# Kernel tuning notes

Hardware: AMD Instinct MI355X
Metric: run time of the kernel (lower is better)

Reference implementation:

```python
import jax, jax.numpy as jnp
import numpy as np

HS = 512; L = 4; T = 128; M = 2048; FF = 2048; NH = 4; DH = HS // NH
STDV = 1.0 / float(np.sqrt(HS))


def setup_inputs() -> dict:
    key = jax.random.key(0)
    ks = iter(jax.random.split(key, 32))

    def u(shape):
        return jax.random.uniform(next(ks), shape, jnp.float32, -STDV, STDV)

    return {
        "x": jax.random.normal(next(ks), (1, T, HS), jnp.float32),
        "historical_states": jax.random.normal(next(ks), (M, L, HS), jnp.float32),
        "Wx": u((L, 3, HS, HS)), "bx": u((L, 3, HS)),
        "Wh": u((L, 3, HS, HS)), "bh": u((L, 3, HS)),
        "sa_Win": u((L, 3 * HS, HS)), "sa_bin": u((L, 3 * HS)),
        "sa_Wo": u((L, HS, HS)), "sa_bo": u((L, HS)),
        "ca_Win": u((L, 3 * HS, HS)), "ca_bin": u((L, 3 * HS)),
        "ca_Wo": u((L, HS, HS)), "ca_bo": u((L, HS)),
        "ff_W1": u((L, FF, HS)), "ff_b1": u((L, FF)),
        "ff_W2": u((L, HS, FF)), "ff_b2": u((L, HS)),
        "ln_g": u((L, 3, HS)), "ln_b": u((L, 3, HS)),
    }


def _layer_norm(v, g, b):
    m = v.mean(-1, keepdims=True)
    var = ((v - m) ** 2).mean(-1, keepdims=True)
    return (v - m) / jnp.sqrt(var + 1e-5) * g + b


def _forward(x, historical_states, Wx, bx, Wh, bh, sa_Win, sa_bin, sa_Wo, sa_bo,
             ca_Win, ca_bin, ca_Wo, ca_bo, ff_W1, ff_b1, ff_W2, ff_b2, ln_g, ln_b):
    n_layers, _, hs, _ = Wx.shape
    # Cross-attn K/V over the static historical memory are time-invariant: precompute once.
    Wk = ca_Win[:, hs:2 * hs, :]; bk = ca_bin[:, hs:2 * hs]
    Wv = ca_Win[:, 2 * hs:, :]; bv = ca_bin[:, 2 * hs:]
    K = (jnp.einsum('mle,lfe->lmf', historical_states, Wk) + bk[:, None, :]).reshape(n_layers, -1, NH, DH)
    V = (jnp.einsum('mle,lfe->lmf', historical_states, Wv) + bv[:, None, :]).reshape(n_layers, -1, NH, DH)
    scale = 1.0 / jnp.sqrt(jnp.asarray(DH, x.dtype))

    def decoder(i, f):
        # post-norm TransformerDecoderLayer, tgt length 1, eval mode (no dropout).
        # Self-attn over a single position: softmax of one logit == 1 -> out = Wo @ (Wv_self f + bv_self) + bo.
        v_sa = sa_Win[i, 2 * hs:] @ f + sa_bin[i, 2 * hs:]
        sa = sa_Wo[i] @ v_sa + sa_bo[i]
        x1 = _layer_norm(f + sa, ln_g[i, 0], ln_b[i, 0])
        q = (ca_Win[i, :hs] @ x1 + ca_bin[i, :hs]).reshape(NH, DH)
        att = jax.nn.softmax(jnp.einsum('hd,mhd->hm', q, K[i]) * scale, axis=-1)
        ctx = jnp.einsum('hm,mhd->hd', att, V[i]).reshape(hs)
        x2 = _layer_norm(x1 + ca_Wo[i] @ ctx + ca_bo[i], ln_g[i, 1], ln_b[i, 1])
        ff = ff_W2[i] @ jax.nn.relu(ff_W1[i] @ x2 + ff_b1[i]) + ff_b2[i]
        return _layer_norm(x2 + ff, ln_g[i, 2], ln_b[i, 2])

    def step(carry, x_t):
        h_prev, c_prev = carry  # (L, HS) each; batch is structurally 1
        xin = x_t
        h_new = []; c_new = []
        for i in range(n_layers):
            z = (jnp.einsum('gij,j->gi', Wx[i], xin) + bx[i]
                 + jnp.einsum('gij,j->gi', Wh[i], h_prev[i]) + bh[i])  # (3, HS)
            i_t = jax.nn.sigmoid(z[0]); f0 = jax.nn.sigmoid(z[1]); g_t = jnp.tanh(z[2])
            f_t = jax.nn.sigmoid(c_prev[i] - decoder(i, f0))
            c_i = f_t * c_prev[i] + i_t * g_t
            xin = jnp.tanh(c_i)
            h_new.append(xin); c_new.append(c_i)
        h = jnp.stack(h_new); c = jnp.stack(c_new)
        return (h, c), h[-1]

    h0 = jnp.zeros((n_layers, hs), x.dtype)
    c0 = jnp.zeros((n_layers, hs), x.dtype)
    (h_T, c_T), hidden = jax.lax.scan(step, (h0, c0), x[0])  # hidden: (T, HS)
    return hidden[None], h_T[:, None, :], c_T[:, None, :]


def reference(x, historical_states, Wx, bx, Wh, bh, sa_Win, sa_bin, sa_Wo, sa_bo,
              ca_Win, ca_bin, ca_Wo, ca_bo, ff_W1, ff_b1, ff_W2, ff_b2, ln_g, ln_b):
    return _forward(x, historical_states, Wx, bx, Wh, bh, sa_Win, sa_bin, sa_Wo, sa_bo,
                    ca_Win, ca_bin, ca_Wo, ca_bo, ff_W1, ff_b1, ff_W2, ff_b2, ln_g, ln_b)
```

## Files before the change

### kernel.cpp

```cpp
#include <hip/hip_runtime.h>

#define HS   512
#define LNUM 4
#define TT   128
#define MMEM 2048
#define FFD  2048
#define NB   256
#define NT   512
#define INV512 (1.0f/512.0f)
#define QSCALE 0.08838834764831845f

constexpr size_t KHALF = (size_t)LNUM*MMEM*HS/2;
constexpr size_t HHALF = (size_t)LNUM*HS*HS/2;
constexpr size_t FHALF = (size_t)LNUM*FFD*HS/2;
constexpr size_t OFF_KBF    = 0;
constexpr size_t OFF_VBF    = OFF_KBF    + KHALF;
constexpr size_t OFF_WCOMBBF= OFF_VBF    + KHALF;
constexpr size_t OFF_WQTBF  = OFF_WCOMBBF+ HHALF;
constexpr size_t OFF_W2TBF  = OFF_WQTBF  + HHALF;
constexpr size_t OFF_FFW1BF = OFF_W2TBF  + FHALF;
constexpr size_t OFF_CAWOBF = OFF_FFW1BF + FHALF;
constexpr size_t OFF_CSA    = OFF_CAWOBF + HHALF;
constexpr size_t OFF_SQ     = OFF_CSA    + (size_t)LNUM*HS;
constexpr size_t OFF_CBQ    = OFF_SQ     + (size_t)LNUM*HS;
constexpr size_t OFF_STATE = OFF_CBQ   + (size_t)LNUM*HS;
constexpr size_t OFF_H     = OFF_STATE;
constexpr size_t OFF_C     = OFF_H     + 2*LNUM*HS;
constexpr size_t OFF_XING  = OFF_C     + 2*LNUM*HS;
constexpr size_t OFF_Z1    = OFF_XING  + HS;
constexpr size_t OFF_Z02   = OFF_Z1    + HS;
constexpr size_t OFF_T2G   = OFF_Z02   + 2*HS;
constexpr size_t OFF_YP    = OFF_T2G   + HS;
constexpr size_t OFF_Y2P   = OFF_YP    + 4*HS;
constexpr size_t OFF_CTXP  = OFF_Y2P   + 8*HS;
constexpr size_t OFF_DENS  = OFF_CTXP  + 8*HS;
constexpr size_t OFF_S1S   = OFF_DENS  + 128;
constexpr size_t OFF_S2S   = OFF_S1S   + 64;
constexpr size_t OFF_J1    = OFF_S2S   + 64;
constexpr size_t OFF_J2    = OFF_J1    + 65*32;
constexpr size_t OFF_FLAGS = OFF_J2    + 128*32;
constexpr size_t WS_TOTAL  = OFF_FLAGS + (size_t)NB*32;

__device__ __forceinline__ float wred(float v) {
#pragma unroll
  for (int m = 32; m; m >>= 1) v += __shfl_xor(v, m);
  return v;
}
__device__ __forceinline__ float sigm(float x) { return 1.0f/(1.0f+__expf(-x)); }

__device__ __forceinline__ unsigned short f2bf(float f) {
  unsigned u = __float_as_uint(f);
  unsigned r = (u + 0x7fffu + ((u >> 16) & 1u)) >> 16;
  return (unsigned short)r;
}
__device__ __forceinline__ float bf2f(unsigned short h) {
  return __uint_as_float(((unsigned)h) << 16);
}

__device__ __forceinline__ float ald(const float* p) {
  return __hip_atomic_load(p, __ATOMIC_RELAXED, __HIP_MEMORY_SCOPE_AGENT);
}
__device__ __forceinline__ void ast(float* p, float v) {
  __hip_atomic_store(p, v, __ATOMIC_RELAXED, __HIP_MEMORY_SCOPE_AGENT);
}
__device__ __forceinline__ unsigned aldu(const unsigned* p) {
  return __hip_atomic_load(p, __ATOMIC_RELAXED, __HIP_MEMORY_SCOPE_AGENT);
}
__device__ __forceinline__ void astu(unsigned* p, unsigned v) {
  __hip_atomic_store(p, v, __ATOMIC_RELAXED, __HIP_MEMORY_SCOPE_AGENT);
}

template <class F>
__device__ __forceinline__ void barrier_pf(unsigned* flags, unsigned g, F&& pf) {
  asm volatile("s_waitcnt vmcnt(0)" ::: "memory");
  __syncthreads();
  if (threadIdx.x == 0) astu(flags + (size_t)blockIdx.x*32, g);
  pf();
  if (threadIdx.x < NB) {
    const unsigned* f = flags + (size_t)threadIdx.x*32;
    while ((int)(aldu(f) - g) < 0) __builtin_amdgcn_s_sleep(2);
  }
  __syncthreads();
}

__device__ __forceinline__ void jflag(unsigned* J, int id, unsigned val) {
  asm volatile("s_waitcnt vmcnt(0)" ::: "memory");
  __syncthreads();
  if (threadIdx.x == 0) astu(J + (size_t)id*32, val);
}
template <class F>
__device__ __forceinline__ void jwait_pf(unsigned* J, int n, unsigned val, F&& pf) {
  pf();
  if (threadIdx.x < n) {
    const unsigned* f = J + (size_t)threadIdx.x*32;
    while ((int)(aldu(f) - val) < 0) __builtin_amdgcn_s_sleep(1);
  }
  __syncthreads();
}

__device__ __forceinline__ void slotred32(const float* slots, float* sh, int o,
                                          int w, int lane) {
  if (w == 0) {
    float a = (lane < 32) ? ald(slots + lane*2) : ald(slots + (lane-32)*2 + 1);
#pragma unroll
    for (int m = 16; m; m >>= 1) a += __shfl_xor(a, m);
    if (lane == 0)  sh[o]   = a;
    if (lane == 32) sh[o+1] = a;
  }
}


__global__ __launch_bounds__(256) void kv_gemm(
    const float* __restrict__ hist, const float* __restrict__ caWin,
    const float* __restrict__ caBin, unsigned short* __restrict__ out, int koff) {
  __shared__ float As[16][64];
  __shared__ float Bs[16][64];
  const int l = blockIdx.z, m0 = blockIdx.x*64, f0 = blockIdx.y*64;
  const int tid = threadIdx.x, tm = tid >> 4, tf = tid & 15;
  float acc[4][4] = {};
  for (int e0 = 0; e0 < HS; e0 += 16) {
#pragma unroll
    for (int it = 0; it < 4; ++it) {
      int idx = tid + it*256, k = idx & 15, mm = idx >> 4;
      As[k][mm] = hist[((size_t)(m0+mm)*LNUM + l)*HS + e0 + k];
      Bs[k][mm] = caWin[((size_t)l*(3*HS) + koff + f0 + mm)*HS + e0 + k];
    }
    __syncthreads();
#pragma unroll
    for (int k = 0; k < 16; ++k) {
      float a[4], b[4];
#pragma unroll
      for (int x = 0; x < 4; ++x) { a[x] = As[k][tm*4+x]; b[x] = Bs[k][tf*4+x]; }
#pragma unroll
      for (int x = 0; x < 4; ++x)
#pragma unroll
        for (int y = 0; y < 4; ++y) acc[x][y] += a[x]*b[y];
    }
    __syncthreads();
  }
#pragma unroll
  for (int x = 0; x < 4; ++x)
#pragma unroll
    for (int y = 0; y < 4; ++y) {
      int m = m0 + tm*4 + x, f = f0 + tf*4 + y;
      out[((size_t)l*MMEM + m)*HS + f] = f2bf(acc[x][y] + caBin[l*(3*HS) + koff + f]);
    }
}

__global__ __launch_bounds__(256) void wcomb_gemm(
    const float* __restrict__ saWo, const float* __restrict__ saWin,
    unsigned short* __restrict__ wcomb) {
  __shared__ float As[16][64];
  __shared__ float Bs[16][64];
  const int l = blockIdx.z, f0 = blockIdx.x*64, j0 = blockIdx.y*64;
  const int tid = threadIdx.x, tm = tid >> 4, tf = tid & 15;
  float acc[4][4] = {};
  for (int e0 = 0; e0 < HS; e0 += 16) {
#pragma unroll
    for (int it = 0; it < 4; ++it) {
      int idx = tid + it*256;
      { int k = idx & 15, ff = idx >> 4;
        As[k][ff] = saWo[((size_t)l*HS + f0+ff)*HS + e0 + k]; }
      { int jj = idx & 63, k = idx >> 6;
        Bs[k][jj] = saWin[((size_t)l*(3*HS) + 2*HS + e0 + k)*HS + j0 + jj]; }
    }
    __syncthreads();
#pragma unroll
    for (int k = 0; k < 16; ++k) {
      float a[4], b[4];
#pragma unroll
      for (int x = 0; x < 4; ++x) { a[x] = As[k][tm*4+x]; b[x] = Bs[k][tf*4+x]; }
#pragma unroll
      for (int x = 0; x < 4; ++x)
#pragma unroll
        for (int y = 0; y < 4; ++y) acc[x][y] += a[x]*b[y];
    }
    __syncthreads();
  }
#pragma unroll
  for (int x = 0; x < 4; ++x)
#pragma unroll
    for (int y = 0; y < 4; ++y)
      wcomb[(size_t)l*HS*HS + (size_t)(f0+tm*4+x)*HS + (j0+tf*4+y)] = f2bf(acc[x][y]);
}

__global__ __launch_bounds__(256) void transpose_scale_bf(
    const float* __restrict__ in, size_t inLS, int R, int C,
    const float* __restrict__ g, size_t gLS,
    unsigned short* __restrict__ out, size_t outLS) {
  __shared__ float tile[32][33];
  const int l = blockIdx.z, e0 = blockIdx.x*32, f0 = blockIdx.y*32;
  const int tx = threadIdx.x & 31, ty = threadIdx.x >> 5;
#pragma unroll
  for (int r = 0; r < 32; r += 8)
    tile[ty+r][tx] = in[(size_t)l*inLS + (size_t)(f0+ty+r)*C + e0 + tx];
  __syncthreads();
#pragma unroll
  for (int r = 0; r < 32; r += 8) {
    int e = e0 + ty + r, f = f0 + tx;
    float s = g ? g[(size_t)l*gLS + e] : 1.0f;
    out[(size_t)l*outLS + (size_t)e*R + f] = f2bf(tile[tx][ty+r] * s);
  }
}

__global__ __launch_bounds__(256) void bf16_copy(
    const float* __restrict__ in, unsigned short* __restrict__ out, size_t n) {
  for (size_t i = (size_t)blockIdx.x*256 + threadIdx.x; i < n; i += (size_t)gridDim.x*256)
    out[i] = f2bf(in[i]);
}

__global__ __launch_bounds__(256) void csa_kernel(
    const float* __restrict__ saWo, const float* __restrict__ sabin,
    const float* __restrict__ sabo, float* __restrict__ csa) {
  const int w = threadIdx.x >> 6, lane = threadIdx.x & 63;
  const int row = blockIdx.x*4 + w;
  const int l = row >> 9, f = row & 511;
  float acc = 0;
#pragma unroll
  for (int k = 0; k < 8; ++k) {
    int e = lane + 64*k;
    acc += saWo[((size_t)l*HS + f)*HS + e] * sabin[l*(3*HS) + 2*HS + e];
  }
  acc = wred(acc);
  if (lane == 0) csa[row] = acc + sabo[l*HS + f];
}

__global__ __launch_bounds__(256) void sqcbq_kernel(
    const float* __restrict__ caWin, const float* __restrict__ caBin,
    const float* __restrict__ lnG, const float* __restrict__ lnB,
    float* __restrict__ sq, float* __restrict__ cbq) {
  const int w = threadIdx.x >> 6, lane = threadIdx.x & 63;
  const int row = blockIdx.x*4 + w;
  const int l = row >> 9, f = row & 511;
  float a1 = 0, a2 = 0;
#pragma unroll
  for (int k = 0; k < 8; ++k) {
    int e = lane + 64*k;
    float wv = caWin[((size_t)l*(3*HS) + f)*HS + e];
    a1 += wv * lnG[l*(3*HS) + e];
    a2 += wv * lnB[l*(3*HS) + e];
  }
  a1 = wred(a1); a2 = wred(a2);
  if (lane == 0) { sq[row] = a1; cbq[row] = a2 + caBin[l*(3*HS) + f]; }
}


__global__ __launch_bounds__(NT, 2) void seq_kernel(
    const float* __restrict__ x,
    const float* __restrict__ Wx,  const float* __restrict__ bx,
    const float* __restrict__ Wh,  const float* __restrict__ bh,
    const float* __restrict__ caBo,
    const float* __restrict__ ffB1,
    const float* __restrict__ ffB2,
    const float* __restrict__ lnG,  const float* __restrict__ lnB,
    float* __restrict__ ws, float* __restrict__ out) {
  const unsigned short* Kb    = (const unsigned short*)(ws + OFF_KBF);
  const unsigned short* Vb    = (const unsigned short*)(ws + OFF_VBF);
  const unsigned short* Wcomb = (const unsigned short*)(ws + OFF_WCOMBBF);
  const unsigned short* WqT   = (const unsigned short*)(ws + OFF_WQTBF);
  const unsigned short* W2T   = (const unsigned short*)(ws + OFF_W2TBF);
  const unsigned short* F1b   = (const unsigned short*)(ws + OFF_FFW1BF);
  const unsigned short* CaWob = (const unsigned short*)(ws + OFF_CAWOBF);
  const float* csag  = ws + OFF_CSA;
  const float* sqg   = ws + OFF_SQ;
  const float* cbqg  = ws + OFF_CBQ;
  float* hG    = ws + OFF_H;
  float* cG    = ws + OFF_C;
  float* xing  = ws + OFF_XING;
  float* z1g   = ws + OFF_Z1;
  float* z02g  = ws + OFF_Z02;
  float* t2g   = ws + OFF_T2G;
  float* Yp    = ws + OFF_YP;
  float* Y2p   = ws + OFF_Y2P;
  float* ctxP  = ws + OFF_CTXP;
  float* denS  = ws + OFF_DENS;
  float* s1s   = ws + OFF_S1S;
  float* s2s   = ws + OFF_S2S;
  unsigned* J1     = (unsigned*)(ws + OFF_J1);
  unsigned* J2     = (unsigned*)(ws + OFF_J2);
  unsigned* bflags = (unsigned*)(ws + OFF_FLAGS);

  __shared__ float sh_xin[HS], sh_h[HS], sh_vec[HS], sh_aux[HS];
  __shared__ float sh_q[128], sh_p[64], sh_t1[16];
  __shared__ float sh_red[24], sh_den[4];

  const int bid = blockIdx.x, tid = threadIdx.x;
  const int w = tid >> 6, lane = tid & 63;
  unsigned gen = 1;

  float pZx[8], pZh[8];
  float pZx2[8], pZh2[8];
  unsigned short pWc[2][8], pWq[16];
  unsigned short pK[8][2], pV[16];
  unsigned short pCa[2][8];
  unsigned short pF1[8], pW2[8];

  auto pfH1 = [&](int l) {
    if (bid < 64) {
      const float* wxr = Wx + (((size_t)l*3 + 1)*HS + bid*8 + w)*HS;
      const float* whr = Wh + (((size_t)l*3 + 1)*HS + bid*8 + w)*HS;
#pragma unroll
      for (int k = 0; k < 8; ++k) { pZx[k] = wxr[lane+64*k]; pZh[k] = whr[lane+64*k]; }
    }
  };
  auto pfH2 = [&](int l) {
    if (bid < 32) {
#pragma unroll
      for (int rr = 0; rr < 2; ++rr) {
        const unsigned short* wr = Wcomb + ((size_t)l*HS + bid*16 + w*2 + rr)*HS;
#pragma unroll
        for (int k = 0; k < 8; ++k) pWc[rr][k] = wr[lane+64*k];
      }
#pragma unroll
      for (int r = 0; r < 16; ++r)
        pWq[r] = WqT[((size_t)l*HS + bid*16 + r)*HS + tid];
    }
  };
  auto pfH3 = [&](int l) {
    if (bid >= 32 && bid < 160) {
      const int b2 = bid - 32, h = b2 >> 5, mseg = b2 & 31;
#pragma unroll
      for (int rr = 0; rr < 8; ++rr) {
        const unsigned short* kr = Kb + ((size_t)l*MMEM + mseg*64 + w*8 + rr)*HS + h*128;
        pK[rr][0] = kr[lane]; pK[rr][1] = kr[lane+64];
      }
#pragma unroll
      for (int ml = 0; ml < 16; ++ml)
        pV[ml] = Vb[((size_t)l*MMEM + mseg*64 + (tid>>7)*16 + ml)*HS + h*128 + (tid & 127)];
    }
  };
  auto pfZ = [&](int l) {
    if (bid < 32 || bid >= 160) {
      const int zb = (bid < 32) ? bid : bid - 128;
      const int rowid = zb*8 + w;
      const int g = (rowid < 512) ? 0 : 2;
      const int f = rowid & 511;
      const float* wxr = Wx + (((size_t)l*3 + g)*HS + f)*HS;
      const float* whr = Wh + (((size_t)l*3 + g)*HS + f)*HS;
#pragma unroll
      for (int k = 0; k < 8; ++k) { pZx2[k] = wxr[lane+64*k]; pZh2[k] = whr[lane+64*k]; }
    }
  };
  auto pfH4 = [&](int l) {
    if (bid < 32) {
#pragma unroll
      for (int rr = 0; rr < 2; ++rr) {
        const unsigned short* wr = CaWob + ((size_t)l*HS + bid*16 + w*2 + rr)*HS;
#pragma unroll
        for (int k = 0; k < 8; ++k) pCa[rr][k] = wr[lane+64*k];
      }
    }
  };
  auto pfH5 = [&](int l) {
    const unsigned short* wr = F1b + ((size_t)l*FFD + bid*8 + w)*HS;
#pragma unroll
    for (int k = 0; k < 8; ++k) pF1[k] = wr[lane+64*k];
#pragma unroll
    for (int r = 0; r < 8; ++r)
      pW2[r] = W2T[((size_t)l*FFD + bid*8 + r)*HS + tid];
  };

  auto do_update = [&](int ip, int parp, float& xn, float& cn) {
    const int j = tid;
    float t2v = ald(t2g + j);
    float z0  = ald(z02g + j);
    float z2  = ald(z02g + HS + j);
    float y2 = 0;
#pragma unroll
    for (int p = 0; p < 8; ++p) y2 += ald(Y2p + (size_t)p*HS + j);
    slotred32(s2s, sh_red, 16, w, lane);
    __syncthreads();
    float m2 = sh_red[16]*INV512;
    float r2 = rsqrtf(sh_red[17]*INV512 - m2*m2 + 1e-5f);
    float x2 = (t2v-m2)*r2*lnG[(ip*3+1)*HS+j] + lnB[(ip*3+1)*HS+j];
    float t3 = x2 + y2 + ffB2[ip*HS + j];
    float s_ = t3, q_ = t3*t3;
#pragma unroll
    for (int m = 32; m; m >>= 1) { s_ += __shfl_xor(s_, m); q_ += __shfl_xor(q_, m); }
    if (lane == 0) { sh_red[w] = s_; sh_red[8+w] = q_; }
    __syncthreads();
    if (tid == 0) {
      float a = 0, b = 0;
#pragma unroll
      for (int k = 0; k < 8; ++k) { a += sh_red[k]; b += sh_red[8+k]; }
      sh_red[0] = a; sh_red[1] = b;
    }
    __syncthreads();
    float m3 = sh_red[0]*INV512;
    float r3 = rsqrtf(sh_red[1]*INV512 - m3*m3 + 1e-5f);
    float d  = (t3-m3)*r3*lnG[(ip*3+2)*HS+j] + lnB[(ip*3+2)*HS+j];
    float cp = ald(cG + (parp*LNUM + ip)*HS + j);
    float ft = sigm(cp - d);
    float it = sigm(z0);
    float gt = tanhf(z2);
    cn = ft*cp + it*gt;
    xn = tanhf(cn);
  };

  pfH1(0); pfH2(0); pfH3(0);

  for (int s = 0; s < TT*LNUM; ++s) {
    const int t = s >> 2, i = s & 3;
    const int par = t & 1;
    const unsigned jv = (unsigned)(s + 1);
    if (bid < 64) {
      float xn = 0.f, cn = 0.f;
      if (s > 0) {
        const int ip = (s-1) & 3, tp = (s-1) >> 2, parp = tp & 1;
        if (bid == 0 || i > 0) {
          do_update(ip, parp, xn, cn);
          if (bid == 0) {
            ast(hG + ((parp^1)*LNUM + ip)*HS + tid, xn);
            ast(cG + ((parp^1)*LNUM + ip)*HS + tid, cn);
            if (ip == 3) out[tp*HS + tid] = xn;
          }
        }
      }
      float xv = (i == 0) ? x[t*HS + tid] : xn;
      sh_xin[tid] = xv;
      sh_h[tid]   = ald(hG + (par*LNUM + i)*HS + tid);
      if (bid == 0) ast(xing + tid, xv);
      __syncthreads();
      const int f = bid*8 + w;
      float acc = 0;
#pragma unroll
      for (int k = 0; k < 8; ++k) {
        int e = lane + 64*k;
        acc += pZx[k]*sh_xin[e] + pZh[k]*sh_h[e];
      }
      acc = wred(acc);
      if (lane == 0) ast(z1g + f, acc + bx[(i*3+1)*HS + f] + bh[(i*3+1)*HS + f]);
      jflag(J1, bid, jv);
    } else if (bid == 64) {
#pragma unroll
      for (int p = 0; p < 4; ++p) ast(Yp + (size_t)p*HS + tid, 0.f);
      jflag(J1, 64, jv);
    } else if (bid == 65) {
#pragma unroll
      for (int p = 0; p < 8; ++p) ast(ctxP + (size_t)p*HS + tid, 0.f);
    } else if (bid == 66) {
      jwait_pf(J1, 65, jv, [&]{});
#pragma unroll
      for (int p = 0; p < 8; ++p) ast(Y2p + (size_t)p*HS + tid, 0.f);
    }
    if (bid < 32) {
      jwait_pf(J1, 65, jv, [&]{});
      sh_vec[tid] = sigm(ald(z1g + tid));
      __syncthreads();
#pragma unroll
      for (int rr = 0; rr < 2; ++rr) {
        const int r = w*2 + rr, j = bid*16 + r;
        float acc = 0;
#pragma unroll
        for (int k = 0; k < 8; ++k) acc += bf2f(pWc[rr][k])*sh_vec[lane + 64*k];
        acc = wred(acc);
        if (lane == 0) {
          float t1v = sh_vec[j] + acc + csag[i*HS + j];
          sh_t1[r]  = t1v;
          sh_aux[r] = t1v;
        }
      }
      __syncthreads();
      {
        float yl = 0;
#pragma unroll
        for (int r = 0; r < 16; ++r) yl += sh_aux[r] * bf2f(pWq[r]);
        atomicAdd(&Yp[(size_t)(bid & 3)*HS + tid], yl);
      }
      if (w == 0 && lane < 16) {
        float v = sh_aux[lane], s_ = v, q_ = v*v;
#pragma unroll
        for (int m = 8; m; m >>= 1) { s_ += __shfl_xor(s_, m); q_ += __shfl_xor(q_, m); }
        if (lane == 0) { ast(s1s + bid*2, s_); ast(s1s + bid*2 + 1, q_); }
      }
    }
    barrier_pf(bflags, gen, [&]{ pfZ(i); pfH4(i); pfH5(i); });
    if (bid >= 32 && bid < 160) {
      const int b2 = bid - 32, h = b2 >> 5, mseg = b2 & 31;
      slotred32(s1s, sh_red, 18, w, lane);
      __syncthreads();
      if (tid < 128) {
        float m1 = sh_red[18]*INV512;
        float r1 = rsqrtf(sh_red[19]*INV512 - m1*m1 + 1e-5f);
        int f = h*128 + tid;
        float Ysum = 0;
#pragma unroll
        for (int p = 0; p < 4; ++p) Ysum += ald(Yp + (size_t)p*HS + f);
        sh_q[tid] = r1*(Ysum - m1*sqg[i*HS + f]) + cbqg[i*HS + f];
      }
      __syncthreads();
#pragma unroll
      for (int rr = 0; rr < 8; ++rr) {
        float acc = sh_q[lane]*bf2f(pK[rr][0]) + sh_q[lane+64]*bf2f(pK[rr][1]);
        acc = wred(acc);
        if (lane == 0) sh_p[w*8 + rr] = __expf(acc * QSCALE);
      }
      __syncthreads();
      {
        const int d = tid & 127, mg = tid >> 7;
        float acc = 0;
#pragma unroll
        for (int ml = 0; ml < 16; ++ml) acc += sh_p[mg*16 + ml] * bf2f(pV[ml]);
        atomicAdd(&ctxP[(size_t)((b2 & 1)*4 + mg)*HS + h*128 + d], acc);
      }
      if (w == 0) {
        float v = wred(sh_p[lane]);
        if (lane == 0) ast(denS + h*32 + mseg, v);
      }
      jflag(J2, b2, jv);
    } else {
      const int zb = (bid < 32) ? bid : bid - 128;
      if (bid >= 160) {
        sh_xin[tid] = ald(xing + tid);
        sh_h[tid]   = ald(hG + (par*LNUM + i)*HS + tid);
      }
      __syncthreads();
      const int rowid = zb*8 + w;
      const int g = (rowid < 512) ? 0 : 2;
      const int f = rowid & 511;
      float acc = 0;
#pragma unroll
      for (int k = 0; k < 8; ++k) {
        int e = lane + 64*k;
        acc += pZx2[k]*sh_xin[e] + pZh2[k]*sh_h[e];
      }
      acc = wred(acc);
      if (lane == 0) ast(z02g + (g ? HS : 0) + f, acc + bx[(i*3+g)*HS + f] + bh[(i*3+g)*HS + f]);
      if (bid < 32) {
        jwait_pf(J2, 128, jv, [&]{});
        slotred32(s1s, sh_red, 18, w, lane);
        if (w >= 4) {
          float v = (lane < 32) ? ald(denS + (w-4)*32 + lane) : 0.f;
#pragma unroll
          for (int m = 16; m; m >>= 1) v += __shfl_xor(v, m);
          if (lane == 0) sh_den[w-4] = v;
        }
        __syncthreads();
        const float m1 = sh_red[18]*INV512;
        const float r1 = rsqrtf(sh_red[19]*INV512 - m1*m1 + 1e-5f);
        {
          float c = 0;
#pragma unroll
          for (int p = 0; p < 8; ++p) c += ald(ctxP + (size_t)p*HS + tid);
          sh_vec[tid] = c / sh_den[tid >> 7];
        }
        __syncthreads();
#pragma unroll
        for (int rr = 0; rr < 2; ++rr) {
          const int r = w*2 + rr, j = bid*16 + r;
          float a2 = 0;
#pragma unroll
          for (int k = 0; k < 8; ++k) a2 += bf2f(pCa[rr][k])*sh_vec[lane + 64*k];
          a2 = wred(a2);
          if (lane == 0) {
            float x1 = (sh_t1[r]-m1)*r1*lnG[(i*3)*HS + j] + lnB[(i*3)*HS + j];
            float t2v = x1 + a2 + caBo[i*HS + j];
            ast(t2g + j, t2v);
            sh_aux[r] = t2v;
          }
        }
        __syncthreads();
        if (w == 0 && lane < 16) {
          float v = sh_aux[lane], s_ = v, q_ = v*v;
#pragma unroll
          for (int m = 8; m; m >>= 1) { s_ += __shfl_xor(s_, m); q_ += __shfl_xor(q_, m); }
          if (lane == 0) { ast(s2s + bid*2, s_); ast(s2s + bid*2 + 1, q_); }
        }
      }
    }
    barrier_pf(bflags, gen+1, [&]{ const int nl = (s+1) & 3; pfH1(nl); pfH2(nl); pfH3(nl); });
    {
      slotred32(s2s, sh_red, 16, w, lane);
      __syncthreads();
      const float m2 = sh_red[16]*INV512;
      const float r2 = rsqrtf(sh_red[17]*INV512 - m2*m2 + 1e-5f);
      sh_vec[tid] = (ald(t2g + tid)-m2)*r2*lnG[(i*3+1)*HS + tid] + lnB[(i*3+1)*HS + tid];
      __syncthreads();
      const int kk = bid*8 + w;
      float acc = 0;
#pragma unroll
      for (int k = 0; k < 8; ++k) acc += bf2f(pF1[k])*sh_vec[lane + 64*k];
      acc = wred(acc);
      if (lane == 0) sh_aux[w] = fmaxf(acc + ffB1[i*FFD + kk], 0.f);
      __syncthreads();
      float yl = 0;
#pragma unroll
      for (int r = 0; r < 8; ++r) yl += sh_aux[r] * bf2f(pW2[r]);
      atomicAdd(&Y2p[(size_t)(bid & 7)*HS + tid], yl);
    }
    barrier_pf(bflags, gen+2, [&]{});
    gen += 3;
  }

  if (bid == 0) {
    float xn, cn;
    do_update(3, 1, xn, cn);
    out[127*HS + tid] = xn;
    out[TT*HS + 3*HS + tid] = xn;
    out[TT*HS + LNUM*HS + 3*HS + tid] = cn;
#pragma unroll
    for (int ii = 0; ii < 3; ++ii) {
      out[TT*HS + ii*HS + tid]            = ald(hG + (0*LNUM + ii)*HS + tid);
      out[TT*HS + LNUM*HS + ii*HS + tid]  = ald(cG + (0*LNUM + ii)*HS + tid);
    }
  }
}

extern "C" void kernel_launch(void* const* d_in, const int* in_sizes, int n_in,
                              void* d_out, int out_size, void* d_ws, size_t ws_size,
                              hipStream_t stream) {
  const float* x      = (const float*)d_in[0];
  const float* hist   = (const float*)d_in[1];
  const float* Wx     = (const float*)d_in[2];
  const float* bx     = (const float*)d_in[3];
  const float* Wh     = (const float*)d_in[4];
  const float* bh     = (const float*)d_in[5];
  const float* saWin  = (const float*)d_in[6];
  const float* saBin  = (const float*)d_in[7];
  const float* saWo   = (const float*)d_in[8];
  const float* saBo   = (const float*)d_in[9];
  const float* caWin  = (const float*)d_in[10];
  const float* caBin  = (const float*)d_in[11];
  const float* caWo   = (const float*)d_in[12];
  const float* caBo   = (const float*)d_in[13];
  const float* ffW1   = (const float*)d_in[14];
  const float* ffB1   = (const float*)d_in[15];
  const float* ffW2   = (const float*)d_in[16];
  const float* ffB2   = (const float*)d_in[17];
  const float* lnG    = (const float*)d_in[18];
  const float* lnB    = (const float*)d_in[19];
  float* ws  = (float*)d_ws;
  float* out = (float*)d_out;

  hipMemsetAsync((char*)d_ws + OFF_STATE*sizeof(float), 0,
                 (WS_TOTAL - OFF_STATE)*sizeof(float), stream);

  kv_gemm<<<dim3(MMEM/64, HS/64, LNUM), 256, 0, stream>>>(
      hist, caWin, caBin, (unsigned short*)(ws + OFF_KBF), HS);
  kv_gemm<<<dim3(MMEM/64, HS/64, LNUM), 256, 0, stream>>>(
      hist, caWin, caBin, (unsigned short*)(ws + OFF_VBF), 2*HS);
  wcomb_gemm<<<dim3(HS/64, HS/64, LNUM), 256, 0, stream>>>(
      saWo, saWin, (unsigned short*)(ws + OFF_WCOMBBF));
  csa_kernel<<<(LNUM*HS)/4, 256, 0, stream>>>(saWo, saBin, saBo, ws + OFF_CSA);
  transpose_scale_bf<<<dim3(HS/32, HS/32, LNUM), 256, 0, stream>>>(
      caWin, (size_t)(3*HS)*HS, HS, HS, lnG, (size_t)(3*HS),
      (unsigned short*)(ws + OFF_WQTBF), (size_t)HS*HS);
  sqcbq_kernel<<<(LNUM*HS)/4, 256, 0, stream>>>(caWin, caBin, lnG, lnB, ws + OFF_SQ, ws + OFF_CBQ);
  transpose_scale_bf<<<dim3(FFD/32, HS/32, LNUM), 256, 0, stream>>>(
      ffW2, (size_t)HS*FFD, HS, FFD, nullptr, 0,
      (unsigned short*)(ws + OFF_W2TBF), (size_t)FFD*HS);
  bf16_copy<<<2048, 256, 0, stream>>>(ffW1, (unsigned short*)(ws + OFF_FFW1BF),
                                      (size_t)LNUM*FFD*HS);
  bf16_copy<<<1024, 256, 0, stream>>>(caWo, (unsigned short*)(ws + OFF_CAWOBF),
                                      (size_t)LNUM*HS*HS);

  seq_kernel<<<NB, NT, 0, stream>>>(x, Wx, bx, Wh, bh, caBo,
                                    ffB1, ffB2, lnG, lnB, ws, out);
}
```

Measured before the change: 13.82 ms.

## Replace per-step grid barriers with sequence-tagged dataflow polling and role-specialized blocks

Restructures the persistent kernel so each block has a fixed role: Z gates, transformer chain, attention with the z0/z2 gates, or FFN. Intermediates move through 64-bit slots tagged with the step number that consumers poll. This removes two of the three grid-wide barriers per step and the atomicAdd-based partial sums, which need zeroing, in favour of per-producer partial slots. Weights are prefetched as packed bf16 pairs, and z0/z2 use double buffering. The cost is more polling traffic, larger register footprints, and more complex ordering reasoning that relies on relaxed atomics.

Result: slower. 24.80 ms (+79.4%).

```diff
diff --git a/kernel.cpp b/kernel.cpp
--- a/kernel.cpp
+++ b/kernel.cpp
@@ -9,6 +9,8 @@
 #define NT   512
 #define INV512 (1.0f/512.0f)
 #define QSCALE 0.08838834764831845f
+
+typedef unsigned long long ull;
 
 constexpr size_t KHALF = (size_t)LNUM*MMEM*HS/2;
 constexpr size_t HHALF = (size_t)LNUM*HS*HS/2;
@@ -23,23 +25,21 @@
 constexpr size_t OFF_CSA    = OFF_CAWOBF + HHALF;
 constexpr size_t OFF_SQ     = OFF_CSA    + (size_t)LNUM*HS;
 constexpr size_t OFF_CBQ    = OFF_SQ     + (size_t)LNUM*HS;
-constexpr size_t OFF_STATE = OFF_CBQ   + (size_t)LNUM*HS;
-constexpr size_t OFF_H     = OFF_STATE;
-constexpr size_t OFF_C     = OFF_H     + 2*LNUM*HS;
-constexpr size_t OFF_XING  = OFF_C     + 2*LNUM*HS;
-constexpr size_t OFF_Z1    = OFF_XING  + HS;
-constexpr size_t OFF_Z02   = OFF_Z1    + HS;
-constexpr size_t OFF_T2G   = OFF_Z02   + 2*HS;
-constexpr size_t OFF_YP    = OFF_T2G   + HS;
-constexpr size_t OFF_Y2P   = OFF_YP    + 4*HS;
-constexpr size_t OFF_CTXP  = OFF_Y2P   + 8*HS;
-constexpr size_t OFF_DENS  = OFF_CTXP  + 8*HS;
-constexpr size_t OFF_S1S   = OFF_DENS  + 128;
-constexpr size_t OFF_S2S   = OFF_S1S   + 64;
-constexpr size_t OFF_J1    = OFF_S2S   + 64;
-constexpr size_t OFF_J2    = OFF_J1    + 65*32;
-constexpr size_t OFF_FLAGS = OFF_J2    + 128*32;
-constexpr size_t WS_TOTAL  = OFF_FLAGS + (size_t)NB*32;
+constexpr size_t OFF_STATE  = OFF_CBQ    + (size_t)LNUM*HS;
+constexpr size_t OFF_H      = OFF_STATE;
+constexpr size_t OFF_C      = OFF_H      + 2*LNUM*HS;
+constexpr size_t OFF_Z02    = OFF_C      + 2*LNUM*HS;
+constexpr size_t OFF_Y2P    = OFF_Z02    + 2*2*HS;
+constexpr size_t OFF_Z1PW   = OFF_Y2P    + 32*HS;
+constexpr size_t OFF_XINPW  = OFF_Z1PW   + 2*HS;
+constexpr size_t OFF_T2PW   = OFF_XINPW  + 2*HS;
+constexpr size_t OFF_YPW    = OFF_T2PW   + 2*HS;
+constexpr size_t OFF_CTXPW  = OFF_YPW    + 2*32*HS;
+constexpr size_t OFF_DENPW  = OFF_CTXPW  + 2*128*128;
+constexpr size_t OFF_S1PW   = OFF_DENPW  + 2*128;
+constexpr size_t OFF_S2PW   = OFF_S1PW   + 2*64;
+constexpr size_t OFF_FLAGS  = OFF_S2PW   + 2*64;
+constexpr size_t WS_TOTAL   = OFF_FLAGS  + (size_t)NB*32;
 
 __device__ __forceinline__ float wred(float v) {
 #pragma unroll
@@ -47,14 +47,14 @@
   return v;
 }
 __device__ __forceinline__ float sigm(float x) { return 1.0f/(1.0f+__expf(-x)); }
-
 __device__ __forceinline__ unsigned short f2bf(float f) {
   unsigned u = __float_as_uint(f);
-  unsigned r = (u + 0x7fffu + ((u >> 16) & 1u)) >> 16;
-  return (unsigned short)r;
-}
-__device__ __forceinline__ float bf2f(unsigned short h) {
-  return __uint_as_float(((unsigned)h) << 16);
+  return (unsigned short)((u + 0x7fffu + ((u >> 16) & 1u)) >> 16);
+}
+__device__ __forceinline__ float bflo(unsigned v){ return __uint_as_float(v << 16); }
+__device__ __forceinline__ float bfhi(unsigned v){ return __uint_as_float(v & 0xffff0000u); }
+__device__ __forceinline__ unsigned ldpack(const unsigned short* a, const unsigned short* b){
+  return (unsigned)(*a) | ((unsigned)(*b) << 16);
 }
 
 __device__ __forceinline__ float ald(const float* p) {
@@ -69,9 +69,43 @@
 __device__ __forceinline__ void astu(unsigned* p, unsigned v) {
   __hip_atomic_store(p, v, __ATOMIC_RELAXED, __HIP_MEMORY_SCOPE_AGENT);
 }
+__device__ __forceinline__ ull aldq(const ull* p) {
+  return __hip_atomic_load(p, __ATOMIC_RELAXED, __HIP_MEMORY_SCOPE_AGENT);
+}
+__device__ __forceinline__ void astq(ull* p, ull v) {
+  __hip_atomic_store(p, v, __ATOMIC_RELAXED, __HIP_MEMORY_SCOPE_AGENT);
+}
+__device__ __forceinline__ void pwst(ull* p, unsigned seq, float v) {
+  astq(p, ((ull)__float_as_uint(v) << 32) | (ull)seq);
+}
+__device__ __forceinline__ float pwpoll(const ull* p, unsigned seq) {
+  ull v = aldq(p);
+  while ((unsigned)v != seq) { __builtin_amdgcn_s_sleep(1); v = aldq(p); }
+  return __uint_as_float((unsigned)(v >> 32));
+}
+__device__ __forceinline__ float pwval(const ull* p) {
+  return ald((const float*)p + 1);
+}
+template <int N>
+__device__ __forceinline__ float pwpollsum(const ull* base, int stride, unsigned seq) {
+  constexpr int C = (N < 16) ? N : 16;
+  float acc = 0;
+  ull v[C];
+#pragma unroll
+  for (int c = 0; c < N; c += C) {
+#pragma unroll
+    for (int p = 0; p < C; ++p) v[p] = aldq(base + (size_t)(c+p)*stride);
+#pragma unroll
+    for (int p = 0; p < C; ++p) {
+      while ((unsigned)v[p] != seq) { __builtin_amdgcn_s_sleep(1); v[p] = aldq(base + (size_t)(c+p)*stride); }
+      acc += __uint_as_float((unsigned)(v[p] >> 32));
+    }
+  }
+  return acc;
+}
 
 template <class F>
-__device__ __forceinline__ void barrier_pf(unsigned* flags, unsigned g, F&& pf) {
+__device__ __forceinline__ void gridbar(unsigned* flags, unsigned g, F&& pf) {
   asm volatile("s_waitcnt vmcnt(0)" ::: "memory");
   __syncthreads();
   if (threadIdx.x == 0) astu(flags + (size_t)blockIdx.x*32, g);
@@ -81,32 +115,6 @@
     while ((int)(aldu(f) - g) < 0) __builtin_amdgcn_s_sleep(2);
   }
   __syncthreads();
-}
-
-__device__ __forceinline__ void jflag(unsigned* J, int id, unsigned val) {
-  asm volatile("s_waitcnt vmcnt(0)" ::: "memory");
-  __syncthreads();
-  if (threadIdx.x == 0) astu(J + (size_t)id*32, val);
-}
-template <class F>
-__device__ __forceinline__ void jwait_pf(unsigned* J, int n, unsigned val, F&& pf) {
-  pf();
-  if (threadIdx.x < n) {
-    const unsigned* f = J + (size_t)threadIdx.x*32;
-    while ((int)(aldu(f) - val) < 0) __builtin_amdgcn_s_sleep(1);
-  }
-  __syncthreads();
-}
-
-__device__ __forceinline__ void slotred32(const float* slots, float* sh, int o,
-                                          int w, int lane) {
-  if (w == 0) {
-    float a = (lane < 32) ? ald(slots + lane*2) : ald(slots + (lane-32)*2 + 1);
-#pragma unroll
-    for (int m = 16; m; m >>= 1) a += __shfl_xor(a, m);
-    if (lane == 0)  sh[o]   = a;
-    if (lane == 32) sh[o+1] = a;
-  }
 }
 
 
@@ -266,109 +274,109 @@
   const float* cbqg  = ws + OFF_CBQ;
   float* hG    = ws + OFF_H;
   float* cG    = ws + OFF_C;
-  float* xing  = ws + OFF_XING;
-  float* z1g   = ws + OFF_Z1;
   float* z02g  = ws + OFF_Z02;
-  float* t2g   = ws + OFF_T2G;
-  float* Yp    = ws + OFF_YP;
-  float* Y2p   = ws + OFF_Y2P;
-  float* ctxP  = ws + OFF_CTXP;
-  float* denS  = ws + OFF_DENS;
-  float* s1s   = ws + OFF_S1S;
-  float* s2s   = ws + OFF_S2S;
-  unsigned* J1     = (unsigned*)(ws + OFF_J1);
-  unsigned* J2     = (unsigned*)(ws + OFF_J2);
+  float* Y2P   = ws + OFF_Y2P;
+  ull* Z1PW   = (ull*)(ws + OFF_Z1PW);
+  ull* XINPW  = (ull*)(ws + OFF_XINPW);
+  ull* T2PW   = (ull*)(ws + OFF_T2PW);
+  ull* YPW    = (ull*)(ws + OFF_YPW);
+  ull* CTXPW  = (ull*)(ws + OFF_CTXPW);
+  ull* DENPW  = (ull*)(ws + OFF_DENPW);
+  ull* S1PW   = (ull*)(ws + OFF_S1PW);
+  ull* S2PW   = (ull*)(ws + OFF_S2PW);
   unsigned* bflags = (unsigned*)(ws + OFF_FLAGS);
 
-  __shared__ float sh_xin[HS], sh_h[HS], sh_vec[HS], sh_aux[HS];
-  __shared__ float sh_q[128], sh_p[64], sh_t1[16];
+  __shared__ float sh_xin[HS], sh_h[HS], sh_vec[HS];
+  __shared__ float sh_aux[64], sh_q[128], sh_p[64], sh_t1[16];
   __shared__ float sh_red[24], sh_den[4];
 
   const int bid = blockIdx.x, tid = threadIdx.x;
   const int w = tid >> 6, lane = tid & 63;
-  unsigned gen = 1;
-
-  float pZx[8], pZh[8];
-  float pZx2[8], pZh2[8];
-  unsigned short pWc[2][8], pWq[16];
-  unsigned short pK[8][2], pV[16];
-  unsigned short pCa[2][8];
-  unsigned short pF1[8], pW2[8];
-
-  auto pfH1 = [&](int l) {
-    if (bid < 64) {
+  const bool isZ = bid < 64;
+  const bool isT = bid >= 64 && bid < 96;
+  const bool isA = bid >= 96 && bid < 224;
+
+  unsigned ph[64];
+  float pf32[16];
+
+  auto pfrole = [&](int l) {
+    if (isZ) {
       const float* wxr = Wx + (((size_t)l*3 + 1)*HS + bid*8 + w)*HS;
       const float* whr = Wh + (((size_t)l*3 + 1)*HS + bid*8 + w)*HS;
 #pragma unroll
-      for (int k = 0; k < 8; ++k) { pZx[k] = wxr[lane+64*k]; pZh[k] = whr[lane+64*k]; }
-    }
-  };
-  auto pfH2 = [&](int l) {
-    if (bid < 32) {
+      for (int k = 0; k < 8; ++k) { pf32[k] = wxr[lane+64*k]; pf32[8+k] = whr[lane+64*k]; }
+    } else if (isT) {
+      const int b = bid - 64;
 #pragma unroll
       for (int rr = 0; rr < 2; ++rr) {
-        const unsigned short* wr = Wcomb + ((size_t)l*HS + bid*16 + w*2 + rr)*HS;
-#pragma unroll
-        for (int k = 0; k < 8; ++k) pWc[rr][k] = wr[lane+64*k];
-      }
-#pragma unroll
-      for (int r = 0; r < 16; ++r)
-        pWq[r] = WqT[((size_t)l*HS + bid*16 + r)*HS + tid];
-    }
-  };
-  auto pfH3 = [&](int l) {
-    if (bid >= 32 && bid < 160) {
-      const int b2 = bid - 32, h = b2 >> 5, mseg = b2 & 31;
+        const unsigned short* base = Wcomb + ((size_t)l*HS + b*16 + w*2 + rr)*HS;
+        const unsigned short* cbase = CaWob + ((size_t)l*HS + b*16 + w*2 + rr)*HS;
+#pragma unroll
+        for (int kk = 0; kk < 4; ++kk) {
+          ph[rr*4+kk]    = ldpack(base + lane + 128*kk,  base + lane + 64 + 128*kk);
+          ph[16+rr*4+kk] = ldpack(cbase + lane + 128*kk, cbase + lane + 64 + 128*kk);
+        }
+      }
+#pragma unroll
+      for (int q = 0; q < 8; ++q)
+        ph[8+q] = ldpack(WqT + ((size_t)l*HS + b*16 + 2*q)*HS + tid,
+                         WqT + ((size_t)l*HS + b*16 + 2*q+1)*HS + tid);
+    } else if (isA) {
+      const int b2 = bid - 96, h = b2 >> 5, ms = b2 & 31;
+      const int g4 = tid >> 7, dd = tid & 127;
 #pragma unroll
       for (int rr = 0; rr < 8; ++rr) {
-        const unsigned short* kr = Kb + ((size_t)l*MMEM + mseg*64 + w*8 + rr)*HS + h*128;
-        pK[rr][0] = kr[lane]; pK[rr][1] = kr[lane+64];
-      }
-#pragma unroll
-      for (int ml = 0; ml < 16; ++ml)
-        pV[ml] = Vb[((size_t)l*MMEM + mseg*64 + (tid>>7)*16 + ml)*HS + h*128 + (tid & 127)];
-    }
-  };
-  auto pfZ = [&](int l) {
-    if (bid < 32 || bid >= 160) {
-      const int zb = (bid < 32) ? bid : bid - 128;
-      const int rowid = zb*8 + w;
-      const int g = (rowid < 512) ? 0 : 2;
-      const int f = rowid & 511;
+        const unsigned short* kr = Kb + ((size_t)l*MMEM + ms*64 + w*8 + rr)*HS + h*128;
+        ph[rr] = ldpack(kr + lane, kr + lane + 64);
+      }
+#pragma unroll
+      for (int q = 0; q < 8; ++q)
+        ph[8+q] = ldpack(Vb + ((size_t)l*MMEM + ms*64 + g4*16 + 2*q)*HS + h*128 + dd,
+                         Vb + ((size_t)l*MMEM + ms*64 + g4*16 + 2*q+1)*HS + h*128 + dd);
+      const int rowid = b2*8 + w, g = (rowid < 512) ? 0 : 2, f = rowid & 511;
       const float* wxr = Wx + (((size_t)l*3 + g)*HS + f)*HS;
       const float* whr = Wh + (((size_t)l*3 + g)*HS + f)*HS;
 #pragma unroll
-      for (int k = 0; k < 8; ++k) { pZx2[k] = wxr[lane+64*k]; pZh2[k] = whr[lane+64*k]; }
+      for (int k = 0; k < 8; ++k) { pf32[k] = wxr[lane+64*k]; pf32[8+k] = whr[lane+64*k]; }
+    } else {
+      const int fb = bid - 224;
+#pragma unroll
+      for (int q = 0; q < 8; ++q) {
+        const unsigned short* base = F1b + ((size_t)l*FFD + fb*64 + w*8 + q)*HS;
+#pragma unroll
+        for (int kk = 0; kk < 4; ++kk)
+          ph[q*4+kk] = ldpack(base + lane + 128*kk, base + lane + 64 + 128*kk);
+      }
+#pragma unroll
+      for (int q = 0; q < 32; ++q)
+        ph[32+q] = ldpack(W2T + ((size_t)l*FFD + fb*64 + 2*q)*HS + tid,
+                          W2T + ((size_t)l*FFD + fb*64 + 2*q+1)*HS + tid);
     }
   };
-  auto pfH4 = [&](int l) {
-    if (bid < 32) {
-#pragma unroll
-      for (int rr = 0; rr < 2; ++rr) {
-        const unsigned short* wr = CaWob + ((size_t)l*HS + bid*16 + w*2 + rr)*HS;
-#pragma unroll
-        for (int k = 0; k < 8; ++k) pCa[rr][k] = wr[lane+64*k];
-      }
-    }
-  };
-  auto pfH5 = [&](int l) {
-    const unsigned short* wr = F1b + ((size_t)l*FFD + bid*8 + w)*HS;
-#pragma unroll
-    for (int k = 0; k < 8; ++k) pF1[k] = wr[lane+64*k];
-#pragma unroll
-    for (int r = 0; r < 8; ++r)
-      pW2[r] = W2T[((size_t)l*FFD + bid*8 + r)*HS + tid];
-  };
-
-  auto do_update = [&](int ip, int parp, float& xn, float& cn) {
+
+  auto do_update = [&](int ip, int parp, int parz, float& xn, float& cn) {
     const int j = tid;
-    float t2v = ald(t2g + j);
-    float z0  = ald(z02g + j);
-    float z2  = ald(z02g + HS + j);
+    float t2v = pwval(T2PW + j);
+    float z0  = ald(z02g + parz*1024 + j);
+    float z2  = ald(z02g + parz*1024 + HS + j);
     float y2 = 0;
-#pragma unroll
-    for (int p = 0; p < 8; ++p) y2 += ald(Y2p + (size_t)p*HS + j);
-    slotred32(s2s, sh_red, 16, w, lane);
+    {
+      float yv[16];
+#pragma unroll
+      for (int c = 0; c < 32; c += 16) {
+#pragma unroll
+        for (int p = 0; p < 16; ++p) yv[p] = ald(Y2P + (size_t)(c+p)*HS + j);
+#pragma unroll
+        for (int p = 0; p < 16; ++p) y2 += yv[p];
+      }
+    }
+    if (w == 0) {
+      float a = (lane < 32) ? pwval(S2PW + lane*2) : pwval(S2PW + (lane-32)*2 + 1);
+#pragma unroll
+      for (int m = 16; m; m >>= 1) a += __shfl_xor(a, m);
+      if (lane == 0)  sh_red[16] = a;
+      if (lane == 32) sh_red[17] = a;
+    }
     __syncthreads();
     float m2 = sh_red[16]*INV512;
     float r2 = rsqrtf(sh_red[17]*INV512 - m2*m2 + 1e-5f);
@@ -397,204 +405,226 @@
     xn = tanhf(cn);
   };
 
-  pfH1(0); pfH2(0); pfH3(0);
+  pfrole(0);
 
   for (int s = 0; s < TT*LNUM; ++s) {
     const int t = s >> 2, i = s & 3;
     const int par = t & 1;
-    const unsigned jv = (unsigned)(s + 1);
-    if (bid < 64) {
+    const unsigned sq = (unsigned)(s + 1);
+
+    if (isZ) {
       float xn = 0.f, cn = 0.f;
-      if (s > 0) {
+      if (s > 0 && (bid == 0 || i > 0)) {
         const int ip = (s-1) & 3, tp = (s-1) >> 2, parp = tp & 1;
-        if (bid == 0 || i > 0) {
-          do_update(ip, parp, xn, cn);
-          if (bid == 0) {
-            ast(hG + ((parp^1)*LNUM + ip)*HS + tid, xn);
-            ast(cG + ((parp^1)*LNUM + ip)*HS + tid, cn);
-            if (ip == 3) out[tp*HS + tid] = xn;
-          }
+        do_update(ip, parp, (s-1) & 1, xn, cn);
+        if (bid == 0) {
+          ast(hG + ((parp^1)*LNUM + ip)*HS + tid, xn);
+          ast(cG + ((parp^1)*LNUM + ip)*HS + tid, cn);
+          if (ip == 3) out[tp*HS + tid] = xn;
         }
       }
       float xv = (i == 0) ? x[t*HS + tid] : xn;
+      if (bid == 0) pwst(XINPW + tid, sq, xv);
       sh_xin[tid] = xv;
       sh_h[tid]   = ald(hG + (par*LNUM + i)*HS + tid);
-      if (bid == 0) ast(xing + tid, xv);
       __syncthreads();
       const int f = bid*8 + w;
       float acc = 0;
 #pragma unroll
       for (int k = 0; k < 8; ++k) {
         int e = lane + 64*k;
-        acc += pZx[k]*sh_xin[e] + pZh[k]*sh_h[e];
+        acc += pf32[k]*sh_xin[e] + pf32[8+k]*sh_h[e];
       }
       acc = wred(acc);
-      if (lane == 0) ast(z1g + f, acc + bx[(i*3+1)*HS + f] + bh[(i*3+1)*HS + f]);
-      jflag(J1, bid, jv);
-    } else if (bid == 64) {
-#pragma unroll
-      for (int p = 0; p < 4; ++p) ast(Yp + (size_t)p*HS + tid, 0.f);
-      jflag(J1, 64, jv);
-    } else if (bid == 65) {
-#pragma unroll
-      for (int p = 0; p < 8; ++p) ast(ctxP + (size_t)p*HS + tid, 0.f);
-    } else if (bid == 66) {
-      jwait_pf(J1, 65, jv, [&]{});
-#pragma unroll
-      for (int p = 0; p < 8; ++p) ast(Y2p + (size_t)p*HS + tid, 0.f);
-    }
-    if (bid < 32) {
-      jwait_pf(J1, 65, jv, [&]{});
-      sh_vec[tid] = sigm(ald(z1g + tid));
+      if (lane == 0) pwst(Z1PW + f, sq, acc + bx[(i*3+1)*HS + f] + bh[(i*3+1)*HS + f]);
+    } else if (isT) {
+      const int b = bid - 64;
+      sh_vec[tid] = sigm(pwpoll(Z1PW + tid, sq));
       __syncthreads();
 #pragma unroll
       for (int rr = 0; rr < 2; ++rr) {
-        const int r = w*2 + rr, j = bid*16 + r;
+        const int j = b*16 + w*2 + rr;
         float acc = 0;
 #pragma unroll
-        for (int k = 0; k < 8; ++k) acc += bf2f(pWc[rr][k])*sh_vec[lane + 64*k];
+        for (int kk = 0; kk < 4; ++kk) {
+          unsigned pw = ph[rr*4+kk];
+          acc += bflo(pw)*sh_vec[lane+128*kk] + bfhi(pw)*sh_vec[lane+64+128*kk];
+        }
         acc = wred(acc);
-        if (lane == 0) {
-          float t1v = sh_vec[j] + acc + csag[i*HS + j];
-          sh_t1[r]  = t1v;
-          sh_aux[r] = t1v;
-        }
+        if (lane == 0) sh_t1[w*2+rr] = sh_vec[j] + acc + csag[i*HS + j];
       }
       __syncthreads();
       {
         float yl = 0;
 #pragma unroll
-        for (int r = 0; r < 16; ++r) yl += sh_aux[r] * bf2f(pWq[r]);
-        atomicAdd(&Yp[(size_t)(bid & 3)*HS + tid], yl);
-      }
+        for (int q = 0; q < 8; ++q) {
+          unsigned pw = ph[8+q];
+          yl += sh_t1[2*q]*bflo(pw) + sh_t1[2*q+1]*bfhi(pw);
+        }
+        pwst(YPW + (size_t)b*512 + tid, sq, yl);
+      }
+      if (w == 0 && lane < 16) {
+        float v = sh_t1[lane], s_ = v, q_ = v*v;
+#pragma unroll
+        for (int m = 8; m; m >>= 1) { s_ += __shfl_xor(s_, m); q_ += __shfl_xor(q_, m); }
+        if (lane == 0) { pwst(S1PW + b*2, sq, s_); pwst(S1PW + b*2 + 1, sq, q_); }
+      }
+      const int hh = tid >> 7, dd = tid & 127;
+      float ctxa = pwpollsum<32>(CTXPW + (size_t)hh*4096 + dd, 128, sq);
+      if (tid < 128) sh_q[tid] = pwpoll(DENPW + tid, sq);
+      if (w == 0) {
+        float a = (lane < 32) ? pwpoll(S1PW + lane*2, sq) : pwpoll(S1PW + (lane-32)*2 + 1, sq);
+#pragma unroll
+        for (int m = 16; m; m >>= 1) a += __shfl_xor(a, m);
+        if (lane == 0)  sh_red[18] = a;
+        if (lane == 32) sh_red[19] = a;
+      }
+      __syncthreads();
+      if (w >= 4) {
+        int h2 = w - 4;
+        if (lane < 32) {
+          float v = sh_q[h2*32 + lane];
+#pragma unroll
+          for (int m = 16; m; m >>= 1) v += __shfl_xor(v, m);
+          if (lane == 0) sh_den[h2] = v;
+        }
+      }
+      __syncthreads();
+      sh_vec[tid] = ctxa / sh_den[hh];
+      __syncthreads();
+      const float m1 = sh_red[18]*INV512;
+      const float r1 = rsqrtf(sh_red[19]*INV512 - m1*m1 + 1e-5f);
+#pragma unroll
+      for (int rr = 0; rr < 2; ++rr) {
+        const int r = w*2 + rr, j = b*16 + r;
+        float a2 = 0;
+#pragma unroll
+        for (int kk = 0; kk < 4; ++kk) {
+          unsigned pw = ph[16+rr*4+kk];
+          a2 += bflo(pw)*sh_vec[lane+128*kk] + bfhi(pw)*sh_vec[lane+64+128*kk];
+        }
+        a2 = wred(a2);
+        if (lane == 0) {
+          float x1 = (sh_t1[r]-m1)*r1*lnG[(i*3)*HS + j] + lnB[(i*3)*HS + j];
+          float t2v = x1 + a2 + caBo[i*HS + j];
+          pwst(T2PW + j, sq, t2v);
+          sh_aux[r] = t2v;
+        }
+      }
+      __syncthreads();
       if (w == 0 && lane < 16) {
         float v = sh_aux[lane], s_ = v, q_ = v*v;
 #pragma unroll
         for (int m = 8; m; m >>= 1) { s_ += __shfl_xor(s_, m); q_ += __shfl_xor(q_, m); }
-        if (lane == 0) { ast(s1s + bid*2, s_); ast(s1s + bid*2 + 1, q_); }
-      }
-    }
-    barrier_pf(bflags, gen, [&]{ pfZ(i); pfH4(i); pfH5(i); });
-    if (bid >= 32 && bid < 160) {
-      const int b2 = bid - 32, h = b2 >> 5, mseg = b2 & 31;
-      slotred32(s1s, sh_red, 18, w, lane);
+        if (lane == 0) { pwst(S2PW + b*2, sq, s_); pwst(S2PW + b*2 + 1, sq, q_); }
+      }
+    } else if (isA) {
+      const int b2 = bid - 96, h = b2 >> 5;
+      const int g4 = tid >> 7, dd = tid & 127;
+      sh_vec[tid] = pwpollsum<8>(YPW + (size_t)(g4*8)*512 + h*128 + dd, 512, sq);
+      if (w == 0) {
+        float a = (lane < 32) ? pwpoll(S1PW + lane*2, sq) : pwpoll(S1PW + (lane-32)*2 + 1, sq);
+#pragma unroll
+        for (int m = 16; m; m >>= 1) a += __shfl_xor(a, m);
+        if (lane == 0)  sh_red[18] = a;
+        if (lane == 32) sh_red[19] = a;
+      }
       __syncthreads();
       if (tid < 128) {
+        float Ysum = sh_vec[tid] + sh_vec[128+tid] + sh_vec[256+tid] + sh_vec[384+tid];
         float m1 = sh_red[18]*INV512;
         float r1 = rsqrtf(sh_red[19]*INV512 - m1*m1 + 1e-5f);
         int f = h*128 + tid;
-        float Ysum = 0;
-#pragma unroll
-        for (int p = 0; p < 4; ++p) Ysum += ald(Yp + (size_t)p*HS + f);
         sh_q[tid] = r1*(Ysum - m1*sqg[i*HS + f]) + cbqg[i*HS + f];
       }
       __syncthreads();
 #pragma unroll
       for (int rr = 0; rr < 8; ++rr) {
-        float acc = sh_q[lane]*bf2f(pK[rr][0]) + sh_q[lane+64]*bf2f(pK[rr][1]);
-        acc = wred(acc);
-        if (lane == 0) sh_p[w*8 + rr] = __expf(acc * QSCALE);
+        unsigned pw = ph[rr];
+        float sc = sh_q[lane]*bflo(pw) + sh_q[lane+64]*bfhi(pw);
+        sc = wred(sc);
+        if (lane == 0) sh_p[w*8+rr] = __expf(sc * QSCALE);
       }
       __syncthreads();
       {
-        const int d = tid & 127, mg = tid >> 7;
         float acc = 0;
 #pragma unroll
-        for (int ml = 0; ml < 16; ++ml) acc += sh_p[mg*16 + ml] * bf2f(pV[ml]);
-        atomicAdd(&ctxP[(size_t)((b2 & 1)*4 + mg)*HS + h*128 + d], acc);
+        for (int q = 0; q < 8; ++q) {
+          unsigned pw = ph[8+q];
+          acc += sh_p[g4*16 + 2*q]*bflo(pw) + sh_p[g4*16 + 2*q+1]*bfhi(pw);
+        }
+        sh_vec[tid] = acc;
       }
       if (w == 0) {
         float v = wred(sh_p[lane]);
-        if (lane == 0) ast(denS + h*32 + mseg, v);
-      }
-      jflag(J2, b2, jv);
+        if (lane == 0) pwst(DENPW + b2, sq, v);
+      }
+      __syncthreads();
+      if (tid < 128) {
+        float tot = sh_vec[tid] + sh_vec[128+tid] + sh_vec[256+tid] + sh_vec[384+tid];
+        pwst(CTXPW + (size_t)b2*128 + tid, sq, tot);
+      }
+      float xv = pwpoll(XINPW + tid, sq);
+      sh_xin[tid] = xv;
+      sh_h[tid]   = ald(hG + (par*LNUM + i)*HS + tid);
+      __syncthreads();
+      {
+        const int rowid = b2*8 + w, g = (rowid < 512) ? 0 : 2, f = rowid & 511;
+        float acc = 0;
+#pragma unroll
+        for (int k = 0; k < 8; ++k) {
+          int e = lane + 64*k;
+          acc += pf32[k]*sh_xin[e] + pf32[8+k]*sh_h[e];
+        }
+        acc = wred(acc);
+        if (lane == 0)
+          ast(z02g + (s & 1)*1024 + (g ? HS : 0) + f,
+              acc + bx[(i*3+g)*HS + f] + bh[(i*3+g)*HS + f]);
+      }
     } else {
-      const int zb = (bid < 32) ? bid : bid - 128;
-      if (bid >= 160) {
-        sh_xin[tid] = ald(xing + tid);
-        sh_h[tid]   = ald(hG + (par*LNUM + i)*HS + tid);
-      }
-      __syncthreads();
-      const int rowid = zb*8 + w;
-      const int g = (rowid < 512) ? 0 : 2;
-      const int f = rowid & 511;
-      float acc = 0;
-#pragma unroll
-      for (int k = 0; k < 8; ++k) {
-        int e = lane + 64*k;
-        acc += pZx2[k]*sh_xin[e] + pZh2[k]*sh_h[e];
-      }
-      acc = wred(acc);
-      if (lane == 0) ast(z02g + (g ? HS : 0) + f, acc + bx[(i*3+g)*HS + f] + bh[(i*3+g)*HS + f]);
-      if (bid < 32) {
-        jwait_pf(J2, 128, jv, [&]{});
-        slotred32(s1s, sh_red, 18, w, lane);
-        if (w >= 4) {
-          float v = (lane < 32) ? ald(denS + (w-4)*32 + lane) : 0.f;
-#pragma unroll
-          for (int m = 16; m; m >>= 1) v += __shfl_xor(v, m);
-          if (lane == 0) sh_den[w-4] = v;
-        }
-        __syncthreads();
-        const float m1 = sh_red[18]*INV512;
-        const float r1 = rsqrtf(sh_red[19]*INV512 - m1*m1 + 1e-5f);
-        {
-          float c = 0;
-#pragma unroll
-          for (int p = 0; p < 8; ++p) c += ald(ctxP + (size_t)p*HS + tid);
-          sh_vec[tid] = c / sh_den[tid >> 7];
-        }
-        __syncthreads();
-#pragma unroll
-        for (int rr = 0; rr < 2; ++rr) {
-          const int r = w*2 + rr, j = bid*16 + r;
-          float a2 = 0;
-#pragma unroll
-          for (int k = 0; k < 8; ++k) a2 += bf2f(pCa[rr][k])*sh_vec[lane + 64*k];
-          a2 = wred(a2);
-          if (lane == 0) {
-            float x1 = (sh_t1[r]-m1)*r1*lnG[(i*3)*HS + j] + lnB[(i*3)*HS + j];
-            float t2v = x1 + a2 + caBo[i*HS + j];
-            ast(t2g + j, t2v);
-            sh_aux[r] = t2v;
-          }
-        }
-        __syncthreads();
-        if (w == 0 && lane < 16) {
-          float v = sh_aux[lane], s_ = v, q_ = v*v;
-#pragma unroll
-          for (int m = 8; m; m >>= 1) { s_ += __shfl_xor(s_, m); q_ += __shfl_xor(q_, m); }
-          if (lane == 0) { ast(s2s + bid*2, s_); ast(s2s + bid*2 + 1, q_); }
-        }
-      }
-    }
-    barrier_pf(bflags, gen+1, [&]{ const int nl = (s+1) & 3; pfH1(nl); pfH2(nl); pfH3(nl); });
-    {
-      slotred32(s2s, sh_red, 16, w, lane);
+      const int fb = bid - 224;
+      float t2v = pwpoll(T2PW + tid, sq);
+      if (w == 0) {
+        float a = (lane < 32) ? pwpoll(S2PW + lane*2, sq) : pwpoll(S2PW + (lane-32)*2 + 1, sq);
+#pragma unroll
+        for (int m = 16; m; m >>= 1) a += __shfl_xor(a, m);
+        if (lane == 0)  sh_red[16] = a;
+        if (lane == 32) sh_red[17] = a;
+      }
       __syncthreads();
       const float m2 = sh_red[16]*INV512;
       const float r2 = rsqrtf(sh_red[17]*INV512 - m2*m2 + 1e-5f);
-      sh_vec[tid] = (ald(t2g + tid)-m2)*r2*lnG[(i*3+1)*HS + tid] + lnB[(i*3+1)*HS + tid];
-      __syncthreads();
-      const int kk = bid*8 + w;
-      float acc = 0;
-#pragma unroll
-      for (int k = 0; k < 8; ++k) acc += bf2f(pF1[k])*sh_vec[lane + 64*k];
-      acc = wred(acc);
-      if (lane == 0) sh_aux[w] = fmaxf(acc + ffB1[i*FFD + kk], 0.f);
-      __syncthreads();
-      float yl = 0;
-#pragma unroll
-      for (int r = 0; r < 8; ++r) yl += sh_aux[r] * bf2f(pW2[r]);
-      atomicAdd(&Y2p[(size_t)(bid & 7)*HS + tid], yl);
-    }
-    barrier_pf(bflags, gen+2, [&]{});
-    gen += 3;
+      sh_vec[tid] = (t2v-m2)*r2*lnG[(i*3+1)*HS + tid] + lnB[(i*3+1)*HS + tid];
+      __syncthreads();
+#pragma unroll
+      for (int q = 0; q < 8; ++q) {
+        const int r = w*8 + q;
+        float acc = 0;
+#pragma unroll
+        for (int kk = 0; kk < 4; ++kk) {
+          unsigned pw = ph[q*4+kk];
+          acc += bflo(pw)*sh_vec[lane+128*kk] + bfhi(pw)*sh_vec[lane+64+128*kk];
+        }
+        acc = wred(acc);
+        if (lane == 0) sh_aux[r] = fmaxf(acc + ffB1[i*FFD + fb*64 + r], 0.f);
+      }
+      __syncthreads();
+      {
+        float yl = 0;
+#pragma unroll
+        for (int q = 0; q < 32; ++q) {
+          unsigned pw = ph[32+q];
+          yl += sh_aux[2*q]*bflo(pw) + sh_aux[2*q+1]*bfhi(pw);
+        }
+        ast(Y2P + (size_t)fb*HS + tid, yl);
+      }
+    }
+    gridbar(bflags, sq, [&]{ pfrole((s+1) & 3); });
   }
 
   if (bid == 0) {
     float xn, cn;
-    do_update(3, 1, xn, cn);
+    do_update(3, 1, 1, xn, cn);
     out[127*HS + tid] = xn;
     out[TT*HS + 3*HS + tid] = xn;
     out[TT*HS + LNUM*HS + 3*HS + tid] = cn;
```
